# Optimization experiments

Hardware: AMD Instinct MI355X
Metric: run time of the kernel (lower is better)

The kernel has to match this reference:

```python
import jax, jax.numpy as jnp
import numpy as np

D_MODEL = 64     # input_dim // 4
D_INNER = 128    # expand * d_model
D_STATE = 16
D_CONV = 4
DT_RANK = 4      # ceil(d_model / 16)
EPS = 1e-5


def layernorm(x, g, b):
    m = x.mean(-1, keepdims=True)
    v = x.var(-1, keepdims=True)
    return (x - m) * jax.lax.rsqrt(v + EPS) * g + b


def mamba(u, W_in, W_conv, b_conv, W_xproj, W_dt, b_dt, A_log, Dp, W_out):
    # u: [B, L, d_model]
    B, L, _ = u.shape
    xz = u @ W_in.T                              # [B, L, 2*d_inner]
    xi, z = xz[..., :D_INNER], xz[..., D_INNER:]
    # depthwise causal conv1d over L
    xp = jnp.pad(xi, ((0, 0), (D_CONV - 1, 0), (0, 0)))
    xc = b_conv + sum(xp[:, k:k + L, :] * W_conv[:, k] for k in range(D_CONV))
    xc = jax.nn.silu(xc)                         # [B, L, d_inner]
    proj = xc @ W_xproj.T                        # [B, L, dt_rank + 2*d_state]
    dtp = proj[..., :DT_RANK]
    Bm = proj[..., DT_RANK:DT_RANK + D_STATE]    # [B, L, d_state]
    Cm = proj[..., DT_RANK + D_STATE:]           # [B, L, d_state]
    dt = jax.nn.softplus(dtp @ W_dt.T + b_dt)    # [B, L, d_inner]
    A = -jnp.exp(A_log)                          # [d_inner, d_state]
    dA = jnp.exp(dt[..., None] * A)              # [B, L, d_inner, d_state]
    dBx = (dt * xc)[..., None] * Bm[:, :, None, :]

    def step(h, t):
        dA_t, dBx_t, C_t = t
        h = dA_t * h + dBx_t                     # [B, d_inner, d_state]
        return h, jnp.einsum('bds,bs->bd', h, C_t)

    h0 = jnp.zeros((B, D_INNER, D_STATE), u.dtype)
    _, ys = jax.lax.scan(step, h0, (dA.transpose(1, 0, 2, 3),
                                    dBx.transpose(1, 0, 2, 3),
                                    Cm.transpose(1, 0, 2)))
    y = ys.transpose(1, 0, 2) + Dp * xc          # [B, L, d_inner]
    y = y * jax.nn.silu(z)
    return y @ W_out.T                           # [B, L, d_model]


def _forward(x, x1, x2, x3, g1, be1, g2, be2, g3, be3, g4, be4, skip_scale,
             W_in, W_conv, b_conv, W_xproj, W_dt, b_dt, A_log, D, W_out):
    Bb, C = x.shape[:2]
    img_dims = x2.shape[2:]
    mparams = (W_in, W_conv, b_conv, W_xproj, W_dt, b_dt, A_log, D, W_out)

    def branch(inp, g, b):
        xf = inp.reshape(Bb, C, -1).transpose(0, 2, 1)   # [B, L, C]
        xn = layernorm(xf, g, b)
        return mamba(xn, *mparams) + skip_scale * xn

    x_mamba = jnp.concatenate([branch(x, g1, be1), branch(x1, g2, be2),
                               branch(x2, g3, be3), branch(x3, g4, be4)], axis=2)
    out = x_mamba.transpose(0, 2, 1).reshape(Bb, 4 * C, *img_dims)
    return out


def setup_inputs():
    key = jax.random.key(0)
    ks = jax.random.split(key, 12)
    f = lambda k, shp, s=1.0: jax.random.normal(k, shp, dtype=jnp.float32) * s
    inp = {
        'x': f(ks[0], (8, 64, 32, 32)),
        'x1': f(ks[1], (8, 64, 32, 32)),
        'x2': f(ks[2], (8, 64, 32, 32)),
        'x3': f(ks[3], (8, 64, 32, 32)),
        'g1': jnp.ones(64), 'be1': jnp.zeros(64),
        'g2': jnp.ones(64), 'be2': jnp.zeros(64),
        'g3': jnp.ones(64), 'be3': jnp.zeros(64),
        'g4': jnp.ones(64), 'be4': jnp.zeros(64),
        'skip_scale': jnp.ones((1,), jnp.float32),
        'W_in': f(ks[4], (2 * D_INNER, D_MODEL), 0.1),
        'W_conv': f(ks[5], (D_INNER, D_CONV), 0.3),
        'b_conv': jnp.zeros(D_INNER),
        'W_xproj': f(ks[6], (DT_RANK + 2 * D_STATE, D_INNER), 0.1),
        'W_dt': f(ks[7], (D_INNER, DT_RANK), 0.1),
        'b_dt': f(ks[8], (D_INNER,), 0.1),
        'A_log': jnp.log(jnp.tile(jnp.arange(1, D_STATE + 1, dtype=jnp.float32), (D_INNER, 1))),
        'D': jnp.ones(D_INNER),
        'W_out': f(ks[9], (D_MODEL, D_INNER), 0.1),
    }
    return inp


def reference(x, x1, x2, x3, g1, be1, g2, be2, g3, be3, g4, be4, skip_scale,
              W_in, W_conv, b_conv, W_xproj, W_dt, b_dt, A_log, D, W_out):
    return _forward(x, x1, x2, x3, g1, be1, g2, be2, g3, be3, g4, be4, skip_scale,
                    W_in, W_conv, b_conv, W_xproj, W_dt, b_dt, A_log, D, W_out)
```

## Files before the change

### kernel.cpp

```cpp
#include <hip/hip_runtime.h>
#include <hip/hip_bf16.h>

#define L2E 1.4426950408889634f
#define LN2 0.6931471805599453f

__device__ __forceinline__ float fexp2(float x) { return __builtin_amdgcn_exp2f(x); }
__device__ __forceinline__ float flog2(float x) { return __builtin_amdgcn_logf(x); }
__device__ __forceinline__ int uniform(int x) { return __builtin_amdgcn_readfirstlane(x); }
__device__ __forceinline__ float sigmoidf_(float v) { return 1.f / (1.f + fexp2(-v * L2E)); }
__device__ __forceinline__ float softplusf_(float t) {
    return (t > 20.f) ? t : LN2 * flog2(1.f + fexp2(t * L2E));
}

constexpr size_t O_M   = 0;
constexpr size_t O_RS  = 32768;
constexpr size_t O_G   = 65536;
constexpr size_t O_Z   = 4259840;
constexpr size_t O_XC  = 8454144;
constexpr size_t O_BM  = 12648448;
constexpr size_t O_CM  = 13172736;
constexpr size_t O_DTP = 13697024;
constexpr size_t O_HP  = 13828096;

__global__ __launch_bounds__(256) void k1_ln_inproj(
    const float* __restrict__ x0, const float* __restrict__ x1,
    const float* __restrict__ x2, const float* __restrict__ x3,
    const float* __restrict__ win,
    const float* __restrict__ g1, const float* __restrict__ be1,
    const float* __restrict__ g2, const float* __restrict__ be2,
    const float* __restrict__ g3, const float* __restrict__ be3,
    const float* __restrict__ g4, const float* __restrict__ be4,
    float* __restrict__ ws)
{
    __shared__ float sX[64 * 68];
    __shared__ float sW[64 * 68];
    __shared__ float sM[64], sR[64];
    int bid = blockIdx.x;
    int seq = bid >> 6, jb = (bid >> 4) & 3, pb = bid & 15;
    int branch = seq >> 3, b = seq & 7;
    int tid = threadIdx.x;
    int lane = tid & 63;
    int wq = uniform(tid >> 6);
    const float* xin = (branch==0)?x0:(branch==1)?x1:(branch==2)?x2:x3;
    const float* gam = (branch==0)?g1:(branch==1)?g2:(branch==2)?g3:g4;
    const float* bet = (branch==0)?be1:(branch==1)?be2:(branch==2)?be3:be4;
    const float* xb = xin + (size_t)b * 65536;

#pragma unroll
    for (int r = 0; r < 16; ++r) {
        int row = r * 4 + wq;
        sX[row * 68 + lane] = xb[(size_t)row * 1024 + pb * 64 + lane];
        sW[lane * 68 + row] = win[(size_t)(jb * 64 + row) * 64 + lane];
    }
    __syncthreads();
    if (tid < 64) {
        float sum = 0.f, sq = 0.f;
#pragma unroll
        for (int c = 0; c < 64; ++c) {
            float v = sX[c * 68 + tid];
            sum += v; sq += v * v;
        }
        float mean = sum * (1.f/64.f);
        float var  = sq * (1.f/64.f) - mean * mean;
        float rs   = rsqrtf(var + 1e-5f);
        sM[tid] = mean; sR[tid] = rs;
        if (jb == 0) {
            ws[O_M  + (size_t)seq * 1024 + pb * 64 + tid] = mean;
            ws[O_RS + (size_t)seq * 1024 + pb * 64 + tid] = rs;
        }
    }
    __syncthreads();
#pragma unroll
    for (int r = 0; r < 16; ++r) {
        int c = r * 4 + wq;
        float v = sX[c * 68 + lane];
        sX[c * 68 + lane] = (v - sM[lane]) * sR[lane] * gam[c] + bet[c];
    }
    __syncthreads();
    int jt = tid >> 4, pt = tid & 15;
    float acc[4][4];
#pragma unroll
    for (int i = 0; i < 4; ++i)
#pragma unroll
        for (int j = 0; j < 4; ++j) acc[i][j] = 0.f;
    for (int c = 0; c < 64; ++c) {
        float4 wv = *(const float4*)&sW[c * 68 + jt * 4];
        float4 xv = *(const float4*)&sX[c * 68 + pt * 4];
        float w[4] = {wv.x, wv.y, wv.z, wv.w};
        float x[4] = {xv.x, xv.y, xv.z, xv.w};
#pragma unroll
        for (int i = 0; i < 4; ++i)
#pragma unroll
            for (int j = 0; j < 4; ++j) acc[i][j] += w[i] * x[j];
    }
    int p0 = pb * 64 + pt * 4;
    float* xi = ws + O_G + (size_t)seq * 131072;
    float* zz = ws + O_Z + (size_t)seq * 131072;
#pragma unroll
    for (int ji = 0; ji < 4; ++ji) {
        int j = jb * 64 + jt * 4 + ji;
        float4 v = make_float4(acc[ji][0], acc[ji][1], acc[ji][2], acc[ji][3]);
        if (j < 128) *(float4*)&xi[(size_t)j * 1024 + p0] = v;
        else         *(float4*)&zz[(size_t)(j - 128) * 1024 + p0] = v;
    }
}

__global__ __launch_bounds__(256) void k2_conv_proj(
    const float* __restrict__ wconv, const float* __restrict__ bconv,
    const float* __restrict__ wxp, float* __restrict__ ws)
{
    __shared__ float sWx[128 * 40];
    __shared__ float sAcc[36 * 64];
    int bid = blockIdx.x;
    int seq = bid >> 4, ptile = bid & 15;
    int tid = threadIdx.x;
    int lane = tid & 63;
    int wq = uniform(tid >> 6);
    int p = ptile * 64 + lane;

    for (int i = tid; i < 36 * 64; i += 256) sAcc[i] = 0.f;
    for (int i = tid; i < 36 * 128; i += 256) {
        int j = i >> 7, d = i & 127;
        sWx[d * 40 + j] = wxp[i];
    }
    __syncthreads();

    const float* xirow = ws + O_G  + (size_t)seq * 131072;
    float*       xcrow = ws + O_XC + (size_t)seq * 131072;
    float acc36[36];
#pragma unroll
    for (int j = 0; j < 36; ++j) acc36[j] = 0.f;

    for (int dd = 0; dd < 32; ++dd) {
        int d = wq * 32 + dd;
        const float* row = xirow + (size_t)d * 1024;
        float4 wc = *(const float4*)&wconv[d * 4];
        float v = bconv[d];
        v += ((p >= 3) ? row[p-3] : 0.f) * wc.x;
        v += ((p >= 2) ? row[p-2] : 0.f) * wc.y;
        v += ((p >= 1) ? row[p-1] : 0.f) * wc.z;
        v += row[p] * wc.w;
        v = v * sigmoidf_(v);
        xcrow[(size_t)d * 1024 + p] = v;
#pragma unroll
        for (int jq = 0; jq < 9; ++jq) {
            float4 w4 = *(const float4*)&sWx[d * 40 + jq * 4];
            acc36[jq*4+0] += v * w4.x;
            acc36[jq*4+1] += v * w4.y;
            acc36[jq*4+2] += v * w4.z;
            acc36[jq*4+3] += v * w4.w;
        }
    }
#pragma unroll
    for (int j = 0; j < 36; ++j) atomicAdd(&sAcc[j * 64 + lane], acc36[j]);
    __syncthreads();
    if (tid < 64) {
        int pp = ptile * 64 + tid;
        float* Bm = ws + O_BM + (size_t)seq * 16384;
        float* Cm = ws + O_CM + (size_t)seq * 16384;
        for (int j = 0; j < 36; ++j) {
            float t = sAcc[j * 64 + tid];
            if (j < 4)       ws[O_DTP + ((size_t)seq * 1024 + pp) * 4 + j] = t;
            else if (j < 20) Bm[(size_t)(j - 4)  * 1024 + pp] = t;
            else             Cm[(size_t)(j - 20) * 1024 + pp] = t;
        }
    }
}

__device__ __forceinline__ void k3_preload(const float* wdt, const float* bdt,
                                           const float* alog, int d0, int s0,
                                           float4& wdt0, float4& wdt1, float& bdt0, float& bdt1,
                                           float* a2)
{
    wdt0 = *(const float4*)(wdt + d0 * 4);
    wdt1 = *(const float4*)(wdt + (d0 + 1) * 4);
    bdt0 = bdt[d0]; bdt1 = bdt[d0 + 1];
    float4 a0 = *(const float4*)(alog + d0 * 16 + s0);
    float4 a1 = *(const float4*)(alog + (d0 + 1) * 16 + s0);
    a2[0] = -fexp2(a0.x * L2E) * L2E; a2[1] = -fexp2(a0.y * L2E) * L2E;
    a2[2] = -fexp2(a0.z * L2E) * L2E; a2[3] = -fexp2(a0.w * L2E) * L2E;
    a2[4] = -fexp2(a1.x * L2E) * L2E; a2[5] = -fexp2(a1.y * L2E) * L2E;
    a2[6] = -fexp2(a1.z * L2E) * L2E; a2[7] = -fexp2(a1.w * L2E) * L2E;
}

__global__ __launch_bounds__(256) void k3a_scan(const float* __restrict__ wdt,
                                                const float* __restrict__ bdt,
                                                const float* __restrict__ alog,
                                                float* __restrict__ ws)
{
    __shared__ float sXC[128 * 33];
    __shared__ __align__(16) float sB[32 * 16];
    __shared__ __align__(16) float sDtp[32 * 4];
    int bid = blockIdx.x;
    int seq = bid >> 5, ch = bid & 31;
    int lb = ch * 32;
    int tid = threadIdx.x;
    int d0 = (tid >> 2) * 2, s0 = (tid & 3) * 4;

    float4 wdt0, wdt1; float bdt0, bdt1; float a2[8];
    k3_preload(wdt, bdt, alog, d0, s0, wdt0, wdt1, bdt0, bdt1, a2);

    const float* xcg = ws + O_XC + (size_t)seq * 131072;
    const float* Bmg = ws + O_BM + (size_t)seq * 16384;
    for (int i = tid; i < 4096; i += 256) {
        int d = i >> 5, li = i & 31;
        sXC[d * 33 + li] = xcg[(size_t)d * 1024 + lb + li];
    }
    for (int i = tid; i < 512; i += 256) {
        int s = i >> 5, li = i & 31;
        sB[li * 16 + s] = Bmg[(size_t)s * 1024 + lb + li];
    }
    if (tid < 128) sDtp[tid] = ws[O_DTP + ((size_t)seq * 1024 + lb + (tid >> 2)) * 4 + (tid & 3)];
    __syncthreads();

    float h[8];
#pragma unroll
    for (int i = 0; i < 8; ++i) h[i] = 0.f;
    float sdt0 = 0.f, sdt1 = 0.f;
    for (int li = 0; li < 32; ++li) {
        float4 q = *(const float4*)&sDtp[li * 4];
        float dt0 = softplusf_(bdt0 + q.x*wdt0.x + q.y*wdt0.y + q.z*wdt0.z + q.w*wdt0.w);
        float dt1 = softplusf_(bdt1 + q.x*wdt1.x + q.y*wdt1.y + q.z*wdt1.z + q.w*wdt1.w);
        float xc0 = sXC[d0 * 33 + li], xc1 = sXC[(d0 + 1) * 33 + li];
        float dx0 = dt0 * xc0, dx1 = dt1 * xc1;
        float4 Bv = *(const float4*)&sB[li * 16 + s0];
        float bv[4] = {Bv.x, Bv.y, Bv.z, Bv.w};
        sdt0 += dt0; sdt1 += dt1;
#pragma unroll
        for (int ss = 0; ss < 4; ++ss) {
            float e0 = fexp2(dt0 * a2[ss]);
            h[ss] = e0 * h[ss] + dx0 * bv[ss];
            float e1 = fexp2(dt1 * a2[4 + ss]);
            h[4 + ss] = e1 * h[4 + ss] + dx1 * bv[ss];
        }
    }
    float* hp = ws + O_HP + (size_t)(seq * 32 + ch) * 4096;
#pragma unroll
    for (int ss = 0; ss < 4; ++ss) {
        hp[d0 * 16 + s0 + ss]            = fexp2(a2[ss] * sdt0);
        hp[(d0 + 1) * 16 + s0 + ss]      = fexp2(a2[4 + ss] * sdt1);
        hp[2048 + d0 * 16 + s0 + ss]     = h[ss];
        hp[2048 + (d0 + 1) * 16 + s0 + ss] = h[4 + ss];
    }
}

__global__ __launch_bounds__(256) void k3b_compose(float* __restrict__ ws)
{
    int seq = blockIdx.x;
    int tid = threadIdx.x;
    int d0 = (tid >> 2) * 2, s0 = (tid & 3) * 4;
    int i0 = d0 * 16 + s0, i1 = (d0 + 1) * 16 + s0;
    float h[8];
#pragma unroll
    for (int i = 0; i < 8; ++i) h[i] = 0.f;
    float* hpb = ws + O_HP + (size_t)seq * 32 * 4096;
    for (int c = 0; c < 32; ++c) {
        float* hp = hpb + (size_t)c * 4096;
        float4 P0 = *(const float4*)&hp[i0];
        float4 P1 = *(const float4*)&hp[i1];
        float4 E0 = *(const float4*)&hp[2048 + i0];
        float4 E1 = *(const float4*)&hp[2048 + i1];
        *(float4*)&hp[i0] = make_float4(h[0], h[1], h[2], h[3]);
        *(float4*)&hp[i1] = make_float4(h[4], h[5], h[6], h[7]);
        h[0] = P0.x * h[0] + E0.x; h[1] = P0.y * h[1] + E0.y;
        h[2] = P0.z * h[2] + E0.z; h[3] = P0.w * h[3] + E0.w;
        h[4] = P1.x * h[4] + E1.x; h[5] = P1.y * h[5] + E1.y;
        h[6] = P1.z * h[6] + E1.z; h[7] = P1.w * h[7] + E1.w;
    }
}

__global__ __launch_bounds__(256) void k3c_scan_y(const float* __restrict__ wdt,
                                                  const float* __restrict__ bdt,
                                                  const float* __restrict__ alog,
                                                  float* __restrict__ ws)
{
    __shared__ float sXC[128 * 33];
    __shared__ float sY[128 * 33];
    __shared__ __align__(16) float sB[32 * 16];
    __shared__ __align__(16) float sC[32 * 16];
    __shared__ __align__(16) float sDtp[32 * 4];
    int bid = blockIdx.x;
    int seq = bid >> 5, ch = bid & 31;
    int lb = ch * 32;
    int tid = threadIdx.x;
    int sq = tid & 3;
    int d0 = (tid >> 2) * 2, s0 = sq * 4;

    float4 wdt0, wdt1; float bdt0, bdt1; float a2[8];
    k3_preload(wdt, bdt, alog, d0, s0, wdt0, wdt1, bdt0, bdt1, a2);

    const float* xcg = ws + O_XC + (size_t)seq * 131072;
    const float* Bmg = ws + O_BM + (size_t)seq * 16384;
    const float* Cmg = ws + O_CM + (size_t)seq * 16384;
    float*       gg  = ws + O_G  + (size_t)seq * 131072;
    for (int i = tid; i < 4096; i += 256) {
        int d = i >> 5, li = i & 31;
        sXC[d * 33 + li] = xcg[(size_t)d * 1024 + lb + li];
    }
    for (int i = tid; i < 512; i += 256) {
        int s = i >> 5, li = i & 31;
        sB[li * 16 + s] = Bmg[(size_t)s * 1024 + lb + li];
        sC[li * 16 + s] = Cmg[(size_t)s * 1024 + lb + li];
    }
    if (tid < 128) sDtp[tid] = ws[O_DTP + ((size_t)seq * 1024 + lb + (tid >> 2)) * 4 + (tid & 3)];

    const float* hp = ws + O_HP + (size_t)(seq * 32 + ch) * 4096;
    float4 H0 = *(const float4*)&hp[d0 * 16 + s0];
    float4 H1 = *(const float4*)&hp[(d0 + 1) * 16 + s0];
    float h[8] = {H0.x, H0.y, H0.z, H0.w, H1.x, H1.y, H1.z, H1.w};
    __syncthreads();

    for (int li = 0; li < 32; ++li) {
        float4 q = *(const float4*)&sDtp[li * 4];
        float dt0 = softplusf_(bdt0 + q.x*wdt0.x + q.y*wdt0.y + q.z*wdt0.z + q.w*wdt0.w);
        float dt1 = softplusf_(bdt1 + q.x*wdt1.x + q.y*wdt1.y + q.z*wdt1.z + q.w*wdt1.w);
        float xc0 = sXC[d0 * 33 + li], xc1 = sXC[(d0 + 1) * 33 + li];
        float dx0 = dt0 * xc0, dx1 = dt1 * xc1;
        float4 Bv = *(const float4*)&sB[li * 16 + s0];
        float4 Cv = *(const float4*)&sC[li * 16 + s0];
        float bv[4] = {Bv.x, Bv.y, Bv.z, Bv.w};
        float cv[4] = {Cv.x, Cv.y, Cv.z, Cv.w};
        float acc0 = 0.f, acc1 = 0.f;
#pragma unroll
        for (int ss = 0; ss < 4; ++ss) {
            float e0 = fexp2(dt0 * a2[ss]);
            h[ss] = e0 * h[ss] + dx0 * bv[ss];
            acc0 += h[ss] * cv[ss];
            float e1 = fexp2(dt1 * a2[4 + ss]);
            h[4 + ss] = e1 * h[4 + ss] + dx1 * bv[ss];
            acc1 += h[4 + ss] * cv[ss];
        }
        acc0 += __shfl_xor(acc0, 1); acc0 += __shfl_xor(acc0, 2);
        acc1 += __shfl_xor(acc1, 1); acc1 += __shfl_xor(acc1, 2);
        if (sq == 0) {
            sY[d0 * 33 + li]       = acc0;
            sY[(d0 + 1) * 33 + li] = acc1;
        }
    }
    __syncthreads();
    for (int i = tid; i < 4096; i += 256) {
        int d = i >> 5, li = i & 31;
        gg[(size_t)d * 1024 + lb + li] = sY[d * 33 + li];
    }
}

__global__ __launch_bounds__(256) void k4_out(
    const float* __restrict__ x0, const float* __restrict__ x1,
    const float* __restrict__ x2, const float* __restrict__ x3,
    const float* __restrict__ g1, const float* __restrict__ be1,
    const float* __restrict__ g2, const float* __restrict__ be2,
    const float* __restrict__ g3, const float* __restrict__ be3,
    const float* __restrict__ g4, const float* __restrict__ be4,
    const float* __restrict__ dpar, const float* __restrict__ woutp,
    const float* __restrict__ skipp, const float* __restrict__ ws,
    float* __restrict__ out)
{
    __shared__ float sG[64 * 68];
    __shared__ float sW[64 * 68];
    int bid = blockIdx.x;
    int seq = bid >> 4, pb = bid & 15;
    int branch = seq >> 3, b = seq & 7;
    int tid = threadIdx.x;
    int lane = tid & 63;
    int wq = uniform(tid >> 6);
    int ct = tid >> 4, pt = tid & 15;

    const float* ys = ws + O_G  + (size_t)seq * 131072;
    const float* zz = ws + O_Z  + (size_t)seq * 131072;
    const float* xc = ws + O_XC + (size_t)seq * 131072;

    float acc[4][4];
#pragma unroll
    for (int i = 0; i < 4; ++i)
#pragma unroll
        for (int j = 0; j < 4; ++j) acc[i][j] = 0.f;

    for (int hf = 0; hf < 2; ++hf) {
#pragma unroll
        for (int r = 0; r < 16; ++r) {
            int row = r * 4 + wq;
            sW[lane * 68 + row] = woutp[(size_t)row * 128 + hf * 64 + lane];
            int d = hf * 64 + row;
            size_t off = (size_t)d * 1024 + pb * 64 + lane;
            float yv = ys[off], zv = zz[off], xcv = xc[off];
            sG[row * 68 + lane] = (yv + dpar[d] * xcv) * (zv * sigmoidf_(zv));
        }
        __syncthreads();
        for (int dl = 0; dl < 64; ++dl) {
            float4 wv = *(const float4*)&sW[dl * 68 + ct * 4];
            float4 gv = *(const float4*)&sG[dl * 68 + pt * 4];
            float w[4] = {wv.x, wv.y, wv.z, wv.w};
            float g[4] = {gv.x, gv.y, gv.z, gv.w};
#pragma unroll
            for (int i = 0; i < 4; ++i)
#pragma unroll
                for (int j = 0; j < 4; ++j) acc[i][j] += w[i] * g[j];
        }
        __syncthreads();
    }

    const float* xin = (branch==0)?x0:(branch==1)?x1:(branch==2)?x2:x3;
    const float* gam = (branch==0)?g1:(branch==1)?g2:(branch==2)?g3:g4;
    const float* bet = (branch==0)?be1:(branch==1)?be2:(branch==2)?be3:be4;
    const float* xb = xin + (size_t)b * 65536;
    int p0 = pb * 64 + pt * 4;
    float skipv = skipp[0];
    float4 m4 = *(const float4*)&ws[O_M  + (size_t)seq * 1024 + p0];
    float4 r4 = *(const float4*)&ws[O_RS + (size_t)seq * 1024 + p0];
    float mm[4] = {m4.x, m4.y, m4.z, m4.w};
    float rr[4] = {r4.x, r4.y, r4.z, r4.w};
#pragma unroll
    for (int ci = 0; ci < 4; ++ci) {
        int c = ct * 4 + ci;
        float4 xv = *(const float4*)&xb[(size_t)c * 1024 + p0];
        float xvv[4] = {xv.x, xv.y, xv.z, xv.w};
        float gc = gam[c], bc = bet[c];
        float o[4];
#pragma unroll
        for (int pi = 0; pi < 4; ++pi) {
            float xn = (xvv[pi] - mm[pi]) * rr[pi] * gc + bc;
            o[pi] = acc[ci][pi] + skipv * xn;
        }
        *(float4*)&out[((size_t)b * 256 + branch * 64 + c) * 1024 + p0] =
            make_float4(o[0], o[1], o[2], o[3]);
    }
}

extern "C" void kernel_launch(void* const* d_in, const int* in_sizes, int n_in,
                              void* d_out, int out_size, void* d_ws, size_t ws_size,
                              hipStream_t stream) {
    float* ws = (float*)d_ws;
    auto f = [&](int i) { return (const float*)d_in[i]; };
    hipLaunchKernelGGL(k1_ln_inproj, dim3(2048), dim3(256), 0, stream,
        f(0), f(1), f(2), f(3), f(13),
        f(4), f(5), f(6), f(7), f(8), f(9), f(10), f(11), ws);
    hipLaunchKernelGGL(k2_conv_proj, dim3(512), dim3(256), 0, stream,
        f(14), f(15), f(16), ws);
    hipLaunchKernelGGL(k3a_scan, dim3(1024), dim3(256), 0, stream, f(17), f(18), f(19), ws);
    hipLaunchKernelGGL(k3b_compose, dim3(32), dim3(256), 0, stream, ws);
    hipLaunchKernelGGL(k3c_scan_y, dim3(1024), dim3(256), 0, stream, f(17), f(18), f(19), ws);
    hipLaunchKernelGGL(k4_out, dim3(512), dim3(256), 0, stream,
        f(0), f(1), f(2), f(3),
        f(4), f(5), f(6), f(7), f(8), f(9), f(10), f(11),
        f(20), f(21), f(12), ws, (float*)d_out);
}
```

Measured before the change: 247.9 us.

## Restructure projection GEMMs to read weights from global and precompute dt per chunk

The in-projection, x-projection and out-projection kernels stop staging transposed weights in shared memory. Each wave now owns a group of output channels and reads the weights directly with wave-uniform float4 loads, so they can be served as scalar or cached loads. The conv kernel stages a haloed tile in LDS instead of doing guarded global reads, and replaces shared-memory atomic reductions with a direct per-wave dot product. The scan kernels precompute softplus(dt) once per chunk into LDS rather than recomputing it per state lane, and the dtp layout becomes channel-major. This cuts LDS traffic, atomics and redundant transcendental work, at the cost of more global and cache weight reads and larger register accumulators.

```diff
diff --git a/kernel.cpp b/kernel.cpp
--- a/kernel.cpp
+++ b/kernel.cpp
@@ -33,7 +33,7 @@
     float* __restrict__ ws)
 {
     __shared__ float sX[64 * 68];
-    __shared__ float sW[64 * 68];
+    __shared__ float sPs[256], sPq[256];
     __shared__ float sM[64], sR[64];
     int bid = blockIdx.x;
     int seq = bid >> 6, jb = (bid >> 4) & 3, pb = bid & 15;
@@ -44,24 +44,30 @@
     const float* xin = (branch==0)?x0:(branch==1)?x1:(branch==2)?x2:x3;
     const float* gam = (branch==0)?g1:(branch==1)?g2:(branch==2)?g3:g4;
     const float* bet = (branch==0)?be1:(branch==1)?be2:(branch==2)?be3:be4;
-    const float* xb = xin + (size_t)b * 65536;
-
-#pragma unroll
-    for (int r = 0; r < 16; ++r) {
-        int row = r * 4 + wq;
-        sX[row * 68 + lane] = xb[(size_t)row * 1024 + pb * 64 + lane];
-        sW[lane * 68 + row] = win[(size_t)(jb * 64 + row) * 64 + lane];
+    const float* xb = xin + (size_t)b * 65536 + pb * 64;
+
+#pragma unroll
+    for (int k = 0; k < 4; ++k) {
+        int i = tid + k * 256;
+        int c = i >> 4, p4 = (i & 15) * 4;
+        *(float4*)&sX[c * 68 + p4] = *(const float4*)&xb[(size_t)c * 1024 + p4];
+    }
+    __syncthreads();
+    {
+        float s = 0.f, q = 0.f;
+#pragma unroll
+        for (int cc = 0; cc < 16; ++cc) {
+            float v = sX[(wq * 16 + cc) * 68 + lane];
+            s += v; q += v * v;
+        }
+        sPs[wq * 64 + lane] = s; sPq[wq * 64 + lane] = q;
     }
     __syncthreads();
     if (tid < 64) {
-        float sum = 0.f, sq = 0.f;
-#pragma unroll
-        for (int c = 0; c < 64; ++c) {
-            float v = sX[c * 68 + tid];
-            sum += v; sq += v * v;
-        }
-        float mean = sum * (1.f/64.f);
-        float var  = sq * (1.f/64.f) - mean * mean;
+        float ss = sPs[tid] + sPs[64 + tid] + sPs[128 + tid] + sPs[192 + tid];
+        float qq = sPq[tid] + sPq[64 + tid] + sPq[128 + tid] + sPq[192 + tid];
+        float mean = ss * (1.f/64.f);
+        float var  = qq * (1.f/64.f) - mean * mean;
         float rs   = rsqrtf(var + 1e-5f);
         sM[tid] = mean; sR[tid] = rs;
         if (jb == 0) {
@@ -70,38 +76,40 @@
         }
     }
     __syncthreads();
-#pragma unroll
-    for (int r = 0; r < 16; ++r) {
-        int c = r * 4 + wq;
-        float v = sX[c * 68 + lane];
-        sX[c * 68 + lane] = (v - sM[lane]) * sR[lane] * gam[c] + bet[c];
-    }
-    __syncthreads();
-    int jt = tid >> 4, pt = tid & 15;
-    float acc[4][4];
-#pragma unroll
-    for (int i = 0; i < 4; ++i)
-#pragma unroll
-        for (int j = 0; j < 4; ++j) acc[i][j] = 0.f;
-    for (int c = 0; c < 64; ++c) {
-        float4 wv = *(const float4*)&sW[c * 68 + jt * 4];
-        float4 xv = *(const float4*)&sX[c * 68 + pt * 4];
-        float w[4] = {wv.x, wv.y, wv.z, wv.w};
-        float x[4] = {xv.x, xv.y, xv.z, xv.w};
-#pragma unroll
-        for (int i = 0; i < 4; ++i)
-#pragma unroll
-            for (int j = 0; j < 4; ++j) acc[i][j] += w[i] * x[j];
-    }
-    int p0 = pb * 64 + pt * 4;
+    {
+        float mean = sM[lane], rs = sR[lane];
+#pragma unroll
+        for (int cc = 0; cc < 16; ++cc) {
+            int c = wq * 16 + cc;
+            float v = sX[c * 68 + lane];
+            sX[c * 68 + lane] = (v - mean) * rs * gam[c] + bet[c];
+        }
+    }
+    __syncthreads();
+    float acc[16];
+#pragma unroll
+    for (int jj = 0; jj < 16; ++jj) acc[jj] = 0.f;
+    int jbase = jb * 64 + wq * 16;
+#pragma unroll 4
+    for (int c4 = 0; c4 < 16; ++c4) {
+        float xv0 = sX[(c4*4+0) * 68 + lane];
+        float xv1 = sX[(c4*4+1) * 68 + lane];
+        float xv2 = sX[(c4*4+2) * 68 + lane];
+        float xv3 = sX[(c4*4+3) * 68 + lane];
+#pragma unroll
+        for (int jj = 0; jj < 16; ++jj) {
+            float4 w4 = *(const float4*)&win[(size_t)(jbase + jj) * 64 + c4 * 4];
+            acc[jj] += xv0*w4.x + xv1*w4.y + xv2*w4.z + xv3*w4.w;
+        }
+    }
     float* xi = ws + O_G + (size_t)seq * 131072;
     float* zz = ws + O_Z + (size_t)seq * 131072;
-#pragma unroll
-    for (int ji = 0; ji < 4; ++ji) {
-        int j = jb * 64 + jt * 4 + ji;
-        float4 v = make_float4(acc[ji][0], acc[ji][1], acc[ji][2], acc[ji][3]);
-        if (j < 128) *(float4*)&xi[(size_t)j * 1024 + p0] = v;
-        else         *(float4*)&zz[(size_t)(j - 128) * 1024 + p0] = v;
+    int col = pb * 64 + lane;
+#pragma unroll
+    for (int jj = 0; jj < 16; ++jj) {
+        int j = jbase + jj;
+        if (j < 128) xi[(size_t)j * 1024 + col] = acc[jj];
+        else         zz[(size_t)(j - 128) * 1024 + col] = acc[jj];
     }
 }
 
@@ -109,72 +117,67 @@
     const float* __restrict__ wconv, const float* __restrict__ bconv,
     const float* __restrict__ wxp, float* __restrict__ ws)
 {
-    __shared__ float sWx[128 * 40];
-    __shared__ float sAcc[36 * 64];
+    __shared__ float sXi[128 * 72];
     int bid = blockIdx.x;
     int seq = bid >> 4, ptile = bid & 15;
     int tid = threadIdx.x;
     int lane = tid & 63;
     int wq = uniform(tid >> 6);
-    int p = ptile * 64 + lane;
-
-    for (int i = tid; i < 36 * 64; i += 256) sAcc[i] = 0.f;
-    for (int i = tid; i < 36 * 128; i += 256) {
-        int j = i >> 7, d = i & 127;
-        sWx[d * 40 + j] = wxp[i];
-    }
-    __syncthreads();
-
-    const float* xirow = ws + O_G  + (size_t)seq * 131072;
-    float*       xcrow = ws + O_XC + (size_t)seq * 131072;
-    float acc36[36];
-#pragma unroll
-    for (int j = 0; j < 36; ++j) acc36[j] = 0.f;
-
+    int p0 = ptile * 64;
+    const float* xig = ws + O_G  + (size_t)seq * 131072 + p0;
+    float*       xcg = ws + O_XC + (size_t)seq * 131072 + p0;
+
+#pragma unroll
+    for (int k = 0; k < 8; ++k) {
+        int i = tid + k * 256;
+        int d = i >> 4, p4 = (i & 15) * 4;
+        *(float4*)&sXi[d * 72 + 4 + p4] = *(const float4*)&xig[(size_t)d * 1024 + p4];
+    }
+    if (tid < 128) {
+        float4 hv = (ptile > 0) ? *(const float4*)&xig[(size_t)tid * 1024 - 4]
+                                : make_float4(0.f, 0.f, 0.f, 0.f);
+        *(float4*)&sXi[tid * 72] = hv;
+    }
+    __syncthreads();
     for (int dd = 0; dd < 32; ++dd) {
         int d = wq * 32 + dd;
-        const float* row = xirow + (size_t)d * 1024;
         float4 wc = *(const float4*)&wconv[d * 4];
         float v = bconv[d];
-        v += ((p >= 3) ? row[p-3] : 0.f) * wc.x;
-        v += ((p >= 2) ? row[p-2] : 0.f) * wc.y;
-        v += ((p >= 1) ? row[p-1] : 0.f) * wc.z;
-        v += row[p] * wc.w;
+        int base = d * 72 + 4 + lane;
+        float a3 = sXi[base - 3], a2v = sXi[base - 2], a1 = sXi[base - 1], a0 = sXi[base];
+        v += a3*wc.x + a2v*wc.y + a1*wc.z + a0*wc.w;
         v = v * sigmoidf_(v);
-        xcrow[(size_t)d * 1024 + p] = v;
-#pragma unroll
-        for (int jq = 0; jq < 9; ++jq) {
-            float4 w4 = *(const float4*)&sWx[d * 40 + jq * 4];
-            acc36[jq*4+0] += v * w4.x;
-            acc36[jq*4+1] += v * w4.y;
-            acc36[jq*4+2] += v * w4.z;
-            acc36[jq*4+3] += v * w4.w;
-        }
-    }
-#pragma unroll
-    for (int j = 0; j < 36; ++j) atomicAdd(&sAcc[j * 64 + lane], acc36[j]);
-    __syncthreads();
-    if (tid < 64) {
-        int pp = ptile * 64 + tid;
-        float* Bm = ws + O_BM + (size_t)seq * 16384;
-        float* Cm = ws + O_CM + (size_t)seq * 16384;
-        for (int j = 0; j < 36; ++j) {
-            float t = sAcc[j * 64 + tid];
-            if (j < 4)       ws[O_DTP + ((size_t)seq * 1024 + pp) * 4 + j] = t;
-            else if (j < 20) Bm[(size_t)(j - 4)  * 1024 + pp] = t;
-            else             Cm[(size_t)(j - 20) * 1024 + pp] = t;
-        }
-    }
-}
-
-__device__ __forceinline__ void k3_preload(const float* wdt, const float* bdt,
-                                           const float* alog, int d0, int s0,
-                                           float4& wdt0, float4& wdt1, float& bdt0, float& bdt1,
-                                           float* a2)
-{
-    wdt0 = *(const float4*)(wdt + d0 * 4);
-    wdt1 = *(const float4*)(wdt + (d0 + 1) * 4);
-    bdt0 = bdt[d0]; bdt1 = bdt[d0 + 1];
+        sXi[base] = v;
+        xcg[(size_t)d * 1024 + lane] = v;
+    }
+    __syncthreads();
+    float acc[9];
+#pragma unroll
+    for (int jj = 0; jj < 9; ++jj) acc[jj] = 0.f;
+    int jbase = wq * 9;
+#pragma unroll 4
+    for (int c4 = 0; c4 < 32; ++c4) {
+        float xv0 = sXi[(c4*4+0) * 72 + 4 + lane];
+        float xv1 = sXi[(c4*4+1) * 72 + 4 + lane];
+        float xv2 = sXi[(c4*4+2) * 72 + 4 + lane];
+        float xv3 = sXi[(c4*4+3) * 72 + 4 + lane];
+#pragma unroll
+        for (int jj = 0; jj < 9; ++jj) {
+            float4 w4 = *(const float4*)&wxp[(size_t)(jbase + jj) * 128 + c4 * 4];
+            acc[jj] += xv0*w4.x + xv1*w4.y + xv2*w4.z + xv3*w4.w;
+        }
+    }
+#pragma unroll
+    for (int jj = 0; jj < 9; ++jj) {
+        int j = jbase + jj;
+        float v = acc[jj];
+        if (j < 4)       ws[O_DTP + ((size_t)seq * 4 + j) * 1024 + p0 + lane] = v;
+        else if (j < 20) ws[O_BM + (size_t)seq * 16384 + (size_t)(j - 4)  * 1024 + p0 + lane] = v;
+        else             ws[O_CM + (size_t)seq * 16384 + (size_t)(j - 20) * 1024 + p0 + lane] = v;
+    }
+}
+
+__device__ __forceinline__ void k3_a2(const float* alog, int d0, int s0, float* a2) {
     float4 a0 = *(const float4*)(alog + d0 * 16 + s0);
     float4 a1 = *(const float4*)(alog + (d0 + 1) * 16 + s0);
     a2[0] = -fexp2(a0.x * L2E) * L2E; a2[1] = -fexp2(a0.y * L2E) * L2E;
@@ -183,63 +186,85 @@
     a2[6] = -fexp2(a1.z * L2E) * L2E; a2[7] = -fexp2(a1.w * L2E) * L2E;
 }
 
+__device__ __forceinline__ void k3_stage(const float* __restrict__ wdt,
+                                         const float* __restrict__ bdt,
+                                         const float* __restrict__ ws,
+                                         int seq, int lb, int tid,
+                                         float* sXC, float* sDt, float* sDtp4, float* sB)
+{
+    const float* xcg = ws + O_XC + (size_t)seq * 131072;
+    const float* Bmg = ws + O_BM + (size_t)seq * 16384;
+    const float* dtp = ws + O_DTP + (size_t)seq * 4096;
+#pragma unroll
+    for (int k = 0; k < 16; ++k) {
+        int i = tid + k * 256;
+        int d = i >> 5, li = i & 31;
+        sXC[d * 33 + li] = xcg[(size_t)d * 1024 + lb + li];
+    }
+#pragma unroll
+    for (int k = 0; k < 2; ++k) {
+        int i = tid + k * 256;
+        int s = i >> 5, li = i & 31;
+        sB[li * 16 + s] = Bmg[(size_t)s * 1024 + lb + li];
+    }
+    if (tid < 128) {
+        int jj = tid >> 5, li = tid & 31;
+        sDtp4[jj * 33 + li] = dtp[(size_t)jj * 1024 + lb + li];
+    }
+    __syncthreads();
+#pragma unroll
+    for (int k = 0; k < 16; ++k) {
+        int i = tid + k * 256;
+        int d = i >> 5, li = i & 31;
+        float4 wv = *(const float4*)&wdt[d * 4];
+        float t = bdt[d] + sDtp4[0*33+li]*wv.x + sDtp4[1*33+li]*wv.y
+                         + sDtp4[2*33+li]*wv.z + sDtp4[3*33+li]*wv.w;
+        sDt[d * 33 + li] = softplusf_(t);
+    }
+    __syncthreads();
+}
+
 __global__ __launch_bounds__(256) void k3a_scan(const float* __restrict__ wdt,
                                                 const float* __restrict__ bdt,
                                                 const float* __restrict__ alog,
                                                 float* __restrict__ ws)
 {
     __shared__ float sXC[128 * 33];
+    __shared__ float sDt[128 * 33];
+    __shared__ float sDtp4[4 * 33];
     __shared__ __align__(16) float sB[32 * 16];
-    __shared__ __align__(16) float sDtp[32 * 4];
     int bid = blockIdx.x;
     int seq = bid >> 5, ch = bid & 31;
     int lb = ch * 32;
     int tid = threadIdx.x;
     int d0 = (tid >> 2) * 2, s0 = (tid & 3) * 4;
 
-    float4 wdt0, wdt1; float bdt0, bdt1; float a2[8];
-    k3_preload(wdt, bdt, alog, d0, s0, wdt0, wdt1, bdt0, bdt1, a2);
-
-    const float* xcg = ws + O_XC + (size_t)seq * 131072;
-    const float* Bmg = ws + O_BM + (size_t)seq * 16384;
-    for (int i = tid; i < 4096; i += 256) {
-        int d = i >> 5, li = i & 31;
-        sXC[d * 33 + li] = xcg[(size_t)d * 1024 + lb + li];
-    }
-    for (int i = tid; i < 512; i += 256) {
-        int s = i >> 5, li = i & 31;
-        sB[li * 16 + s] = Bmg[(size_t)s * 1024 + lb + li];
-    }
-    if (tid < 128) sDtp[tid] = ws[O_DTP + ((size_t)seq * 1024 + lb + (tid >> 2)) * 4 + (tid & 3)];
-    __syncthreads();
+    float a2[8];
+    k3_a2(alog, d0, s0, a2);
+    k3_stage(wdt, bdt, ws, seq, lb, tid, sXC, sDt, sDtp4, sB);
 
     float h[8];
 #pragma unroll
     for (int i = 0; i < 8; ++i) h[i] = 0.f;
     float sdt0 = 0.f, sdt1 = 0.f;
     for (int li = 0; li < 32; ++li) {
-        float4 q = *(const float4*)&sDtp[li * 4];
-        float dt0 = softplusf_(bdt0 + q.x*wdt0.x + q.y*wdt0.y + q.z*wdt0.z + q.w*wdt0.w);
-        float dt1 = softplusf_(bdt1 + q.x*wdt1.x + q.y*wdt1.y + q.z*wdt1.z + q.w*wdt1.w);
-        float xc0 = sXC[d0 * 33 + li], xc1 = sXC[(d0 + 1) * 33 + li];
-        float dx0 = dt0 * xc0, dx1 = dt1 * xc1;
+        float dt0 = sDt[d0 * 33 + li], dt1 = sDt[(d0 + 1) * 33 + li];
+        float dx0 = dt0 * sXC[d0 * 33 + li], dx1 = dt1 * sXC[(d0 + 1) * 33 + li];
         float4 Bv = *(const float4*)&sB[li * 16 + s0];
         float bv[4] = {Bv.x, Bv.y, Bv.z, Bv.w};
         sdt0 += dt0; sdt1 += dt1;
 #pragma unroll
         for (int ss = 0; ss < 4; ++ss) {
-            float e0 = fexp2(dt0 * a2[ss]);
-            h[ss] = e0 * h[ss] + dx0 * bv[ss];
-            float e1 = fexp2(dt1 * a2[4 + ss]);
-            h[4 + ss] = e1 * h[4 + ss] + dx1 * bv[ss];
+            h[ss]     = fexp2(dt0 * a2[ss])     * h[ss]     + dx0 * bv[ss];
+            h[4 + ss] = fexp2(dt1 * a2[4 + ss]) * h[4 + ss] + dx1 * bv[ss];
         }
     }
     float* hp = ws + O_HP + (size_t)(seq * 32 + ch) * 4096;
 #pragma unroll
     for (int ss = 0; ss < 4; ++ss) {
-        hp[d0 * 16 + s0 + ss]            = fexp2(a2[ss] * sdt0);
-        hp[(d0 + 1) * 16 + s0 + ss]      = fexp2(a2[4 + ss] * sdt1);
-        hp[2048 + d0 * 16 + s0 + ss]     = h[ss];
+        hp[d0 * 16 + s0 + ss]              = fexp2(a2[ss] * sdt0);
+        hp[(d0 + 1) * 16 + s0 + ss]        = fexp2(a2[4 + ss] * sdt1);
+        hp[2048 + d0 * 16 + s0 + ss]       = h[ss];
         hp[2048 + (d0 + 1) * 16 + s0 + ss] = h[4 + ss];
     }
 }
@@ -275,10 +300,10 @@
                                                   float* __restrict__ ws)
 {
     __shared__ float sXC[128 * 33];
-    __shared__ float sY[128 * 33];
+    __shared__ float sDt[128 * 33];
+    __shared__ float sDtp4[4 * 33];
     __shared__ __align__(16) float sB[32 * 16];
     __shared__ __align__(16) float sC[32 * 16];
-    __shared__ __align__(16) float sDtp[32 * 4];
     int bid = blockIdx.x;
     int seq = bid >> 5, ch = bid & 31;
     int lb = ch * 32;
@@ -286,36 +311,27 @@
     int sq = tid & 3;
     int d0 = (tid >> 2) * 2, s0 = sq * 4;
 
-    float4 wdt0, wdt1; float bdt0, bdt1; float a2[8];
-    k3_preload(wdt, bdt, alog, d0, s0, wdt0, wdt1, bdt0, bdt1, a2);
-
-    const float* xcg = ws + O_XC + (size_t)seq * 131072;
-    const float* Bmg = ws + O_BM + (size_t)seq * 16384;
-    const float* Cmg = ws + O_CM + (size_t)seq * 16384;
-    float*       gg  = ws + O_G  + (size_t)seq * 131072;
-    for (int i = tid; i < 4096; i += 256) {
-        int d = i >> 5, li = i & 31;
-        sXC[d * 33 + li] = xcg[(size_t)d * 1024 + lb + li];
-    }
-    for (int i = tid; i < 512; i += 256) {
-        int s = i >> 5, li = i & 31;
-        sB[li * 16 + s] = Bmg[(size_t)s * 1024 + lb + li];
-        sC[li * 16 + s] = Cmg[(size_t)s * 1024 + lb + li];
-    }
-    if (tid < 128) sDtp[tid] = ws[O_DTP + ((size_t)seq * 1024 + lb + (tid >> 2)) * 4 + (tid & 3)];
+    float a2[8];
+    k3_a2(alog, d0, s0, a2);
+    {
+        const float* Cmg = ws + O_CM + (size_t)seq * 16384;
+#pragma unroll
+        for (int k = 0; k < 2; ++k) {
+            int i = tid + k * 256;
+            int s = i >> 5, li = i & 31;
+            sC[li * 16 + s] = Cmg[(size_t)s * 1024 + lb + li];
+        }
+    }
+    k3_stage(wdt, bdt, ws, seq, lb, tid, sXC, sDt, sDtp4, sB);
 
     const float* hp = ws + O_HP + (size_t)(seq * 32 + ch) * 4096;
     float4 H0 = *(const float4*)&hp[d0 * 16 + s0];
     float4 H1 = *(const float4*)&hp[(d0 + 1) * 16 + s0];
     float h[8] = {H0.x, H0.y, H0.z, H0.w, H1.x, H1.y, H1.z, H1.w};
-    __syncthreads();
 
     for (int li = 0; li < 32; ++li) {
-        float4 q = *(const float4*)&sDtp[li * 4];
-        float dt0 = softplusf_(bdt0 + q.x*wdt0.x + q.y*wdt0.y + q.z*wdt0.z + q.w*wdt0.w);
-        float dt1 = softplusf_(bdt1 + q.x*wdt1.x + q.y*wdt1.y + q.z*wdt1.z + q.w*wdt1.w);
-        float xc0 = sXC[d0 * 33 + li], xc1 = sXC[(d0 + 1) * 33 + li];
-        float dx0 = dt0 * xc0, dx1 = dt1 * xc1;
+        float dt0 = sDt[d0 * 33 + li], dt1 = sDt[(d0 + 1) * 33 + li];
+        float dx0 = dt0 * sXC[d0 * 33 + li], dx1 = dt1 * sXC[(d0 + 1) * 33 + li];
         float4 Bv = *(const float4*)&sB[li * 16 + s0];
         float4 Cv = *(const float4*)&sC[li * 16 + s0];
         float bv[4] = {Bv.x, Bv.y, Bv.z, Bv.w};
@@ -323,24 +339,25 @@
         float acc0 = 0.f, acc1 = 0.f;
 #pragma unroll
         for (int ss = 0; ss < 4; ++ss) {
-            float e0 = fexp2(dt0 * a2[ss]);
-            h[ss] = e0 * h[ss] + dx0 * bv[ss];
+            h[ss] = fexp2(dt0 * a2[ss]) * h[ss] + dx0 * bv[ss];
             acc0 += h[ss] * cv[ss];
-            float e1 = fexp2(dt1 * a2[4 + ss]);
-            h[4 + ss] = e1 * h[4 + ss] + dx1 * bv[ss];
+            h[4 + ss] = fexp2(dt1 * a2[4 + ss]) * h[4 + ss] + dx1 * bv[ss];
             acc1 += h[4 + ss] * cv[ss];
         }
         acc0 += __shfl_xor(acc0, 1); acc0 += __shfl_xor(acc0, 2);
         acc1 += __shfl_xor(acc1, 1); acc1 += __shfl_xor(acc1, 2);
         if (sq == 0) {
-            sY[d0 * 33 + li]       = acc0;
-            sY[(d0 + 1) * 33 + li] = acc1;
-        }
-    }
-    __syncthreads();
-    for (int i = tid; i < 4096; i += 256) {
+            sXC[d0 * 33 + li]       = acc0;
+            sXC[(d0 + 1) * 33 + li] = acc1;
+        }
+    }
+    __syncthreads();
+    float* gg = ws + O_G + (size_t)seq * 131072;
+#pragma unroll
+    for (int k = 0; k < 16; ++k) {
+        int i = tid + k * 256;
         int d = i >> 5, li = i & 31;
-        gg[(size_t)d * 1024 + lb + li] = sY[d * 33 + li];
+        gg[(size_t)d * 1024 + lb + li] = sXC[d * 33 + li];
     }
 }
 
@@ -355,74 +372,64 @@
     const float* __restrict__ skipp, const float* __restrict__ ws,
     float* __restrict__ out)
 {
-    __shared__ float sG[64 * 68];
-    __shared__ float sW[64 * 68];
+    __shared__ float sG[128 * 68];
     int bid = blockIdx.x;
     int seq = bid >> 4, pb = bid & 15;
     int branch = seq >> 3, b = seq & 7;
     int tid = threadIdx.x;
     int lane = tid & 63;
     int wq = uniform(tid >> 6);
-    int ct = tid >> 4, pt = tid & 15;
-
-    const float* ys = ws + O_G  + (size_t)seq * 131072;
-    const float* zz = ws + O_Z  + (size_t)seq * 131072;
-    const float* xc = ws + O_XC + (size_t)seq * 131072;
-
-    float acc[4][4];
-#pragma unroll
-    for (int i = 0; i < 4; ++i)
-#pragma unroll
-        for (int j = 0; j < 4; ++j) acc[i][j] = 0.f;
-
-    for (int hf = 0; hf < 2; ++hf) {
-#pragma unroll
-        for (int r = 0; r < 16; ++r) {
-            int row = r * 4 + wq;
-            sW[lane * 68 + row] = woutp[(size_t)row * 128 + hf * 64 + lane];
-            int d = hf * 64 + row;
-            size_t off = (size_t)d * 1024 + pb * 64 + lane;
-            float yv = ys[off], zv = zz[off], xcv = xc[off];
-            sG[row * 68 + lane] = (yv + dpar[d] * xcv) * (zv * sigmoidf_(zv));
-        }
-        __syncthreads();
-        for (int dl = 0; dl < 64; ++dl) {
-            float4 wv = *(const float4*)&sW[dl * 68 + ct * 4];
-            float4 gv = *(const float4*)&sG[dl * 68 + pt * 4];
-            float w[4] = {wv.x, wv.y, wv.z, wv.w};
-            float g[4] = {gv.x, gv.y, gv.z, gv.w};
-#pragma unroll
-            for (int i = 0; i < 4; ++i)
-#pragma unroll
-                for (int j = 0; j < 4; ++j) acc[i][j] += w[i] * g[j];
-        }
-        __syncthreads();
-    }
-
+    const float* ys = ws + O_G  + (size_t)seq * 131072 + pb * 64;
+    const float* zz = ws + O_Z  + (size_t)seq * 131072 + pb * 64;
+    const float* xc = ws + O_XC + (size_t)seq * 131072 + pb * 64;
+
+#pragma unroll
+    for (int k = 0; k < 8; ++k) {
+        int i = tid + k * 256;
+        int d = i >> 4, p4 = (i & 15) * 4;
+        size_t off = (size_t)d * 1024 + p4;
+        float4 y4 = *(const float4*)&ys[off];
+        float4 z4 = *(const float4*)&zz[off];
+        float4 c4 = *(const float4*)&xc[off];
+        float Dd = dpar[d];
+        float4 g4v;
+        g4v.x = (y4.x + Dd * c4.x) * (z4.x * sigmoidf_(z4.x));
+        g4v.y = (y4.y + Dd * c4.y) * (z4.y * sigmoidf_(z4.y));
+        g4v.z = (y4.z + Dd * c4.z) * (z4.z * sigmoidf_(z4.z));
+        g4v.w = (y4.w + Dd * c4.w) * (z4.w * sigmoidf_(z4.w));
+        *(float4*)&sG[d * 68 + p4] = g4v;
+    }
+    __syncthreads();
+    float acc[16];
+#pragma unroll
+    for (int cc = 0; cc < 16; ++cc) acc[cc] = 0.f;
+    int cbase = wq * 16;
+#pragma unroll 4
+    for (int d4 = 0; d4 < 32; ++d4) {
+        float xv0 = sG[(d4*4+0) * 68 + lane];
+        float xv1 = sG[(d4*4+1) * 68 + lane];
+        float xv2 = sG[(d4*4+2) * 68 + lane];
+        float xv3 = sG[(d4*4+3) * 68 + lane];
+#pragma unroll
+        for (int cc = 0; cc < 16; ++cc) {
+            float4 w4 = *(const float4*)&woutp[(size_t)(cbase + cc) * 128 + d4 * 4];
+            acc[cc] += xv0*w4.x + xv1*w4.y + xv2*w4.z + xv3*w4.w;
+        }
+    }
     const float* xin = (branch==0)?x0:(branch==1)?x1:(branch==2)?x2:x3;
     const float* gam = (branch==0)?g1:(branch==1)?g2:(branch==2)?g3:g4;
     const float* bet = (branch==0)?be1:(branch==1)?be2:(branch==2)?be3:be4;
-    const float* xb = xin + (size_t)b * 65536;
-    int p0 = pb * 64 + pt * 4;
+    const float* xb = xin + (size_t)b * 65536 + pb * 64;
+    int col = pb * 64 + lane;
     float skipv = skipp[0];
-    float4 m4 = *(const float4*)&ws[O_M  + (size_t)seq * 1024 + p0];
-    float4 r4 = *(const float4*)&ws[O_RS + (size_t)seq * 1024 + p0];
-    float mm[4] = {m4.x, m4.y, m4.z, m4.w};
-    float rr[4] = {r4.x, r4.y, r4.z, r4.w};
-#pragma unroll
-    for (int ci = 0; ci < 4; ++ci) {
-        int c = ct * 4 + ci;
-        float4 xv = *(const float4*)&xb[(size_t)c * 1024 + p0];
-        float xvv[4] = {xv.x, xv.y, xv.z, xv.w};
-        float gc = gam[c], bc = bet[c];
-        float o[4];
-#pragma unroll
-        for (int pi = 0; pi < 4; ++pi) {
-            float xn = (xvv[pi] - mm[pi]) * rr[pi] * gc + bc;
-            o[pi] = acc[ci][pi] + skipv * xn;
-        }
-        *(float4*)&out[((size_t)b * 256 + branch * 64 + c) * 1024 + p0] =
-            make_float4(o[0], o[1], o[2], o[3]);
+    float mean = ws[O_M  + (size_t)seq * 1024 + col];
+    float rs   = ws[O_RS + (size_t)seq * 1024 + col];
+#pragma unroll
+    for (int cc = 0; cc < 16; ++cc) {
+        int c = cbase + cc;
+        float xv = xb[(size_t)c * 1024 + lane];
+        float xn = (xv - mean) * rs * gam[c] + bet[c];
+        out[((size_t)b * 256 + branch * 64 + c) * 1024 + col] = acc[cc] + skipv * xn;
     }
 }
 
```

Measured after the change: 267.4 us. 7.9% more time.
